# Kernel tuning notes

Hardware: AMD Instinct MI355X
Metric: run time of the kernel (lower is better)

Reference implementation:

```python
import jax, jax.numpy as jnp
import numpy as np

B, T, NF, C, H, TOPK = 4, 8, 8192, 384, 12, 32
D = C // H
SCALE = D ** -0.5  # qk_scale=None -> head_dim**-0.5


def setup_inputs() -> dict:
    key = jax.random.key(0)
    ks = jax.random.split(key, 4)
    x = jax.random.normal(ks[0], (B, T + NF, C), jnp.float32)
    qs_w = jax.random.normal(ks[1], (T, C, C), jnp.float32) * (C ** -0.5)
    kv_w = jax.random.normal(ks[2], (C, 2 * C), jnp.float32) * (C ** -0.5)
    experts_w = jax.random.normal(ks[3], (T, C, C), jnp.float32) * (C ** -0.5)
    return {"x": x, "qs_w": qs_w, "kv_w": kv_w, "experts_w": experts_w}


def reference(x, qs_w, kv_w, experts_w):
    # x: [B, T+NF, C]; first T tokens are task tokens, rest are feature tokens
    feature = x[:, T:, :]                                          # [B,NF,C]
    kv = (feature @ kv_w).reshape(B, NF, 2, H, D)                  # out dim splits [2,H,D]
    k = kv[:, :, 0].transpose(0, 2, 1, 3)                          # [B,H,NF,D]
    v = kv[:, :, 1].transpose(0, 2, 1, 3)                          # [B,H,NF,D]
    # per-task query linears (no bias), one task token each
    q = jnp.einsum('btc,tco->bto', x[:, :T, :], qs_w)              # [B,T,C]
    q = q.reshape(B, T, H, D).transpose(0, 2, 1, 3)                # [B,H,T,D]
    attn = jnp.einsum('bhtd,bhnd->bhtn', q, k) * SCALE             # [B,H,T,NF]
    vals, idx = jax.lax.top_k(attn, TOPK)                          # [B,H,T,K]
    w = jax.nn.softmax(vals, axis=-1)                              # softmax over top-k only
    # attn_token = (scatter(topk softmax) @ v) == weighted gather of v rows
    v_g = jnp.take_along_axis(v[:, :, None], idx[..., None], axis=3)   # [B,H,T,K,D]
    attn_token = jnp.einsum('bhtk,bhtkd->bhtd', w, v_g)
    attn_token = attn_token.transpose(0, 2, 1, 3).reshape(B, T, C)     # [B,T,C]
    # gather raw feature tokens at top-k indices, weight, scatter into padded zeros
    fm = feature.reshape(B, NF, H, D).transpose(0, 2, 1, 3)        # [B,H,NF,D]
    f_g = jnp.take_along_axis(fm[:, :, None], idx[..., None], axis=3) * w[..., None]  # [B,H,T,K,D]
    bi = jnp.arange(B)[:, None, None, None]
    hi = jnp.arange(H)[None, :, None, None]
    ti = jnp.arange(T)[None, None, :, None]
    # topk indices are unique per row -> set is well-defined
    feature_pad = jnp.zeros((B, H, T, NF, D), x.dtype).at[bi, hi, ti, idx].set(f_g)
    feature_pad = feature_pad.transpose(0, 2, 3, 1, 4).reshape(B, T, NF, C)  # [B,T,NF,C]
    # per-task expert linears; einsum with ones weight == sum over tasks
    feature_out = jnp.einsum('btnc,tco->bno', feature_pad, experts_w)  # [B,NF,C]
    token_out = jnp.einsum('btc,tco->bto', attn_token, experts_w)      # [B,T,C]
    return jnp.concatenate([token_out, feature_out], axis=1)          # [B,T+NF,C]
```

## Files before the change

### kernel.cpp

```cpp
#include <hip/hip_runtime.h>
#include <math.h>

#define B 4
#define T 8
#define NF 8192
#define C 384
#define H 12
#define TOPK 32
#define D 32
#define STOT (T + NF)
#define R (H * T)
#define KSEL 48
#define SCALE 0.17677669529663687f

typedef unsigned int uint;
typedef unsigned short ushort;
typedef short bf16x8 __attribute__((ext_vector_type(8)));
typedef float f32x4 __attribute__((ext_vector_type(4)));

__device__ __forceinline__ uint pk_bf16(float a, float b) {
  uint ua = __builtin_bit_cast(uint, a);
  uint ub = __builtin_bit_cast(uint, b);
  ua = (ua + 0x7FFFu + ((ua >> 16) & 1u)) >> 16;
  ub = (ub + 0x7FFFu + ((ub >> 16) & 1u)) >> 16;
  return ua | (ub << 16);
}

__device__ __forceinline__ ushort f32_key(float s) {
  uint u = __builtin_bit_cast(uint, s);
  uint ub = (u + 0x7FFFu + ((u >> 16) & 1u)) >> 16;
  ub ^= (ub & 0x8000u) ? 0xFFFFu : 0x8000u;
  return (ushort)ub;
}

__global__ __launch_bounds__(256) void ta_qproj_kernel(
    const float* __restrict__ x, const float* __restrict__ qs_w,
    float* __restrict__ q_part) {
  int t = blockIdx.x;
  int o0 = blockIdx.y * 64;
  int z = blockIdx.z;
  int tid = threadIdx.x;
  int o = tid & 63, ks = tid >> 6;
  __shared__ float xs[B][192];
  __shared__ float part[4][B][64];
  if (tid < 192) {
    int b = tid / 48, j4 = (tid % 48) * 4;
    *reinterpret_cast<float4*>(&xs[b][j4]) =
        *reinterpret_cast<const float4*>(x + ((size_t)b * STOT + t) * C + z * 192 + j4);
  }
  __syncthreads();
  float a0 = 0.f, a1 = 0.f, a2 = 0.f, a3 = 0.f;
  const float* w = qs_w + (size_t)t * C * C + (size_t)(z * 192 + ks * 48) * C + o0 + o;
#pragma unroll 8
  for (int c = 0; c < 48; ++c) {
    float wv = w[(size_t)c * C];
    int cj = ks * 48 + c;
    a0 += xs[0][cj] * wv;
    a1 += xs[1][cj] * wv;
    a2 += xs[2][cj] * wv;
    a3 += xs[3][cj] * wv;
  }
  part[ks][0][o] = a0; part[ks][1][o] = a1;
  part[ks][2][o] = a2; part[ks][3][o] = a3;
  __syncthreads();
  {
    int b = tid >> 6, oo = tid & 63;
    float s = part[0][b][oo] + part[1][b][oo] + part[2][b][oo] + part[3][b][oo];
    q_part[(((size_t)z * B + b) * T + t) * C + o0 + oo] = s;
  }
}

__global__ __launch_bounds__(384) void ta_fold_kernel(
    const float* __restrict__ q_part, const float* __restrict__ kv_w,
    float* __restrict__ qk_f32, ushort* __restrict__ qk_bf) {
  int b = blockIdx.x / H, h = blockIdx.x % H;
  int tid = threadIdx.x;
  __shared__ float kS[C][33];
  __shared__ float qh[T][D];
  if (tid < T * D) {
    int t = tid >> 5, d = tid & 31;
    qh[t][d] = q_part[((size_t)b * T + t) * C + h * D + d] +
               q_part[(((size_t)B + b) * T + t) * C + h * D + d];
  }
  for (int j = tid; j < C * 8; j += 384) {
    int c = j >> 3, d4 = (j & 7) * 4;
    float4 v = *reinterpret_cast<const float4*>(
        kv_w + (size_t)c * (2 * C) + h * D + d4);
    kS[c][d4 + 0] = v.x; kS[c][d4 + 1] = v.y;
    kS[c][d4 + 2] = v.z; kS[c][d4 + 3] = v.w;
  }
  __syncthreads();
  float acc[T] = {0.f, 0.f, 0.f, 0.f, 0.f, 0.f, 0.f, 0.f};
#pragma unroll
  for (int d = 0; d < D; ++d) {
    float kv = kS[tid][d];
#pragma unroll
    for (int t = 0; t < T; ++t) acc[t] += qh[t][d] * kv;
  }
#pragma unroll
  for (int t = 0; t < T; ++t) {
    size_t off = ((size_t)b * R + (size_t)h * T + t) * C + tid;
    float a = acc[t];
    qk_f32[off] = a;
    uint ua = __builtin_bit_cast(uint, a);
    qk_bf[off] = (ushort)((ua + 0x7FFFu + ((ua >> 16) & 1u)) >> 16);
  }
}

__global__ __launch_bounds__(256) void ta_scores_kernel(
    const float* __restrict__ x, const ushort* __restrict__ qk_bf,
    ushort* __restrict__ keys) {
  int b = blockIdx.y;
  int n0 = blockIdx.x * 64;
  int tid = threadIdx.x;
  int lane = tid & 63, w = tid >> 6;
  int row16 = lane & 15, kg = lane >> 4;
  __shared__ ushort fS[64][72];
  __shared__ ushort qS[96][72];
  f32x4 acc[6];
#pragma unroll
  for (int i = 0; i < 6; ++i) acc[i] = (f32x4){0.f, 0.f, 0.f, 0.f};

  const float* xb = x + ((size_t)b * STOT + T + n0) * C;
  const ushort* qb = qk_bf + (size_t)b * R * C;

  int frow = tid >> 2, fcg = (tid & 3) * 8;

#pragma unroll 1
  for (int c0 = 0; c0 < C; c0 += 32) {
    {
      const float* src = xb + (size_t)frow * C + c0 + fcg;
      float4 v0 = *reinterpret_cast<const float4*>(src);
      float4 v1 = *reinterpret_cast<const float4*>(src + 4);
      uint4 p;
      p.x = pk_bf16(v0.x, v0.y);
      p.y = pk_bf16(v0.z, v0.w);
      p.z = pk_bf16(v1.x, v1.y);
      p.w = pk_bf16(v1.z, v1.w);
      *reinterpret_cast<uint4*>(&fS[frow][fcg]) = p;
    }
#pragma unroll
    for (int s = 0; s < 2; ++s) {
      int u = tid + 256 * s;
      if (u < 384) {
        int row = u >> 2, cg = (u & 3) * 8;
        uint4 v = *reinterpret_cast<const uint4*>(qb + (size_t)row * C + c0 + cg);
        *reinterpret_cast<uint4*>(&qS[row][cg]) = v;
      }
    }
    __syncthreads();
    bf16x8 bfr = *reinterpret_cast<const bf16x8*>(&fS[w * 16 + row16][kg * 8]);
#pragma unroll
    for (int i = 0; i < 6; ++i) {
      bf16x8 afr = *reinterpret_cast<const bf16x8*>(&qS[i * 16 + row16][kg * 8]);
      acc[i] = __builtin_amdgcn_mfma_f32_16x16x32_bf16(afr, bfr, acc[i], 0, 0, 0);
    }
    __syncthreads();
  }
  int n = n0 + w * 16 + row16;
#pragma unroll
  for (int i = 0; i < 6; ++i) {
    int rbase = i * 16 + kg * 4;
#pragma unroll
    for (int reg = 0; reg < 4; ++reg) {
      keys[((size_t)b * R + rbase + reg) * NF + n] = f32_key(acc[i][reg] * SCALE);
    }
  }
}

__global__ __launch_bounds__(384) void ta_selres_kernel(
    const ushort* __restrict__ keys, const float* __restrict__ x,
    const float* __restrict__ qk_f32, float* __restrict__ w_buf,
    int* __restrict__ idx_buf) {
  int rr = blockIdx.x;
  int b = rr / R;
  int tid = threadIdx.x;
  __shared__ __align__(16) ushort su[NF];
  __shared__ uint hist[256], cum[256];
  __shared__ uint sh_prefix, sh_above, cgt, ceq;
  __shared__ int gt_list[KSEL];
  __shared__ int eq_list[128];
  __shared__ int il[KSEL];
  __shared__ float sv[KSEL];
  __shared__ int rkS[KSEL];
  __shared__ float qS[C];
  __shared__ float smax, esum;

  {
    const uint4* src = reinterpret_cast<const uint4*>(keys + (size_t)rr * NF);
    uint4* dst = reinterpret_cast<uint4*>(su);
    for (int j = tid; j < NF / 8; j += 384) dst[j] = src[j];
  }
  qS[tid] = qk_f32[(size_t)rr * C + tid];
  if (tid < 256) hist[tid] = 0;
  if (tid == 0) { cgt = 0; ceq = 0; }
  __syncthreads();

  for (int i = tid; i < NF; i += 384) atomicAdd(&hist[su[i] >> 8], 1u);
  __syncthreads();
  if (tid < 256) cum[tid] = hist[tid];
  __syncthreads();
#pragma unroll
  for (int off = 1; off < 256; off <<= 1) {
    uint add = (tid < 256 - off) ? cum[tid + off] : 0u;
    __syncthreads();
    if (tid < 256) cum[tid] += add;
    __syncthreads();
  }
  if (tid < 256) {
    uint ge = cum[tid], gn = (tid < 255) ? cum[tid + 1] : 0u;
    if (ge >= (uint)KSEL && gn < (uint)KSEL) { sh_prefix = (uint)tid; sh_above = gn; }
  }
  __syncthreads();
  uint pref1 = sh_prefix, ab1 = sh_above;
  if (tid < 256) hist[tid] = 0;
  __syncthreads();
  for (int i = tid; i < NF; i += 384) {
    uint u = su[i];
    if ((u >> 8) == pref1) atomicAdd(&hist[u & 255], 1u);
  }
  __syncthreads();
  if (tid < 256) cum[tid] = hist[tid];
  __syncthreads();
#pragma unroll
  for (int off = 1; off < 256; off <<= 1) {
    uint add = (tid < 256 - off) ? cum[tid + off] : 0u;
    __syncthreads();
    if (tid < 256) cum[tid] += add;
    __syncthreads();
  }
  {
    uint need2 = (uint)KSEL - ab1;
    if (tid < 256) {
      uint ge = cum[tid], gn = (tid < 255) ? cum[tid + 1] : 0u;
      if (ge >= need2 && gn < need2) {
        sh_prefix = (pref1 << 8) | (uint)tid;
        sh_above = ab1 + gn;
      }
    }
  }
  __syncthreads();
  uint piv = sh_prefix, ab = sh_above;
  for (int i = tid; i < NF; i += 384) {
    uint u = su[i];
    if (u > piv) {
      uint s = atomicAdd(&cgt, 1u);
      gt_list[s] = i;
    } else if (u == piv) {
      uint s = atomicAdd(&ceq, 1u);
      if (s < 128) eq_list[s] = i;
    }
  }
  __syncthreads();
  if (tid < (int)ab) il[tid] = gt_list[tid];
  {
    uint ne = ceq < 128u ? ceq : 128u;
    if (tid < (int)ne) {
      int my = eq_list[tid];
      int r2 = 0;
      for (uint e = 0; e < ne; ++e) r2 += (eq_list[e] < my);
      if (r2 < (int)((uint)KSEL - ab)) il[ab + r2] = my;
    }
  }
  __syncthreads();

  int k = tid >> 3, j = tid & 7;
  const float* fp = x + ((size_t)b * STOT + T + il[k]) * C + j;
  float s = 0.f;
#pragma unroll 8
  for (int m = 0; m < 48; ++m) s += fp[m * 8] * qS[j + m * 8];
  s += __shfl_down(s, 4);
  s += __shfl_down(s, 2);
  s += __shfl_down(s, 1);
  if (j == 0) sv[k] = s * SCALE;
  __syncthreads();
  if (tid < KSEL) {
    float mys = sv[tid];
    int myn = il[tid];
    int r = 0;
#pragma unroll
    for (int e = 0; e < KSEL; ++e) {
      float se = sv[e];
      r += (se > mys) || (se == mys && il[e] < myn);
    }
    rkS[tid] = r;
    if (r == 0) smax = mys;
  }
  __syncthreads();
  float e = 0.f;
  if (tid < KSEL && rkS[tid] < TOPK) e = expf(sv[tid] - smax);
  if (tid < 64) {
    float t2 = e;
#pragma unroll
    for (int off = 32; off; off >>= 1) t2 += __shfl_down(t2, off);
    if (tid == 0) esum = t2;
  }
  __syncthreads();
  if (tid < KSEL && rkS[tid] < TOPK) {
    w_buf[(size_t)rr * TOPK + rkS[tid]] = e / esum;
    idx_buf[(size_t)rr * TOPK + rkS[tid]] = il[tid];
  }
}

__global__ __launch_bounds__(256) void ta_zero_kernel(
    float4* __restrict__ out4, int n4) {
  int i = blockIdx.x * 256 + threadIdx.x;
  int stride = gridDim.x * 256;
  float4 z = {0.f, 0.f, 0.f, 0.f};
  for (int j = i; j < n4; j += stride) out4[j] = z;
}

__global__ __launch_bounds__(256) void ta_gv_kernel(
    const float* __restrict__ x, const float* __restrict__ kv_w,
    const float* __restrict__ w_buf, const int* __restrict__ idx_buf,
    float* __restrict__ g_buf, float* __restrict__ att_buf) {
  int br = blockIdx.x;
  int h = (br / T) % H, b = br / R;
  int tid = threadIdx.x;
  int k = tid >> 3, dg = tid & 7;
  __shared__ float Fc[TOPK][100];
  __shared__ float Vc[96][36];
  __shared__ float vS[TOPK][36];
  __shared__ float wl[TOPK];
  __shared__ int il[TOPK];

  if (tid < TOPK) {
    wl[tid] = w_buf[(size_t)br * TOPK + tid];
    il[tid] = idx_buf[(size_t)br * TOPK + tid];
  }
  __syncthreads();
  float4 acc = {0.f, 0.f, 0.f, 0.f};
  int hc = (h * D) / 96;
#pragma unroll 1
  for (int ch = 0; ch < 4; ++ch) {
    int c0 = ch * 96;
    if (ch) __syncthreads();
#pragma unroll
    for (int s = 0; s < 3; ++s) {
      int u = tid + 256 * s;
      int kr = u / 24, c4 = (u % 24) * 4;
      *reinterpret_cast<float4*>(&Fc[kr][c4]) =
          *reinterpret_cast<const float4*>(
              x + ((size_t)b * STOT + T + il[kr]) * C + c0 + c4);
    }
#pragma unroll
    for (int s = 0; s < 3; ++s) {
      int u = tid + 256 * s;
      int cr = u >> 3, d4 = (u & 7) * 4;
      *reinterpret_cast<float4*>(&Vc[cr][d4]) =
          *reinterpret_cast<const float4*>(
              kv_w + (size_t)(c0 + cr) * (2 * C) + C + h * D + d4);
    }
    __syncthreads();
    if (ch == hc) {
      int off = h * D - c0;
      float4 f = *reinterpret_cast<const float4*>(&Fc[k][off + 4 * dg]);
      float wk = wl[k];
      float4 g = {wk * f.x, wk * f.y, wk * f.z, wk * f.w};
      *reinterpret_cast<float4*>(
          &g_buf[((size_t)br * TOPK + k) * D + 4 * dg]) = g;
    }
#pragma unroll 4
    for (int c = 0; c < 96; c += 4) {
      float4 f4 = *reinterpret_cast<const float4*>(&Fc[k][c]);
      float4 v0 = *reinterpret_cast<const float4*>(&Vc[c + 0][4 * dg]);
      float4 v1 = *reinterpret_cast<const float4*>(&Vc[c + 1][4 * dg]);
      float4 v2 = *reinterpret_cast<const float4*>(&Vc[c + 2][4 * dg]);
      float4 v3 = *reinterpret_cast<const float4*>(&Vc[c + 3][4 * dg]);
      acc.x += f4.x * v0.x + f4.y * v1.x + f4.z * v2.x + f4.w * v3.x;
      acc.y += f4.x * v0.y + f4.y * v1.y + f4.z * v2.y + f4.w * v3.y;
      acc.z += f4.x * v0.z + f4.y * v1.z + f4.z * v2.z + f4.w * v3.z;
      acc.w += f4.x * v0.w + f4.y * v1.w + f4.z * v2.w + f4.w * v3.w;
    }
  }
  *reinterpret_cast<float4*>(&vS[k][4 * dg]) = acc;
  __syncthreads();
  if (tid < D) {
    float a = 0.f;
#pragma unroll
    for (int kk = 0; kk < TOPK; ++kk) a += wl[kk] * vS[kk][tid];
    att_buf[(size_t)br * D + tid] = a;
  }
}

__global__ __launch_bounds__(384) void ta_scatter_kernel(
    const float* __restrict__ ew, const float* __restrict__ g_buf,
    const float* __restrict__ att_buf, const int* __restrict__ idx_buf,
    float* __restrict__ out) {
  int grp = blockIdx.x >> 2, b = blockIdx.x & 3;
  int t = grp / H, h = grp % H;
  int br = b * R + h * T + t;
  int tid = threadIdx.x;
  __shared__ float gS[TOPK * D];
  __shared__ __align__(16) float attS[D];
  __shared__ int ilS[TOPK];

  for (int u = tid; u < TOPK * D / 4; u += 384)
    *reinterpret_cast<float4*>(gS + u * 4) =
        *reinterpret_cast<const float4*>(g_buf + (size_t)br * TOPK * D + u * 4);
  if (tid < TOPK) ilS[tid] = idx_buf[(size_t)br * TOPK + tid];
  if (tid < D) attS[tid] = att_buf[(size_t)br * D + tid];
  __syncthreads();

  float ewc[D];
  const float* ewt = ew + (size_t)t * C * C + (size_t)h * D * C + tid;
#pragma unroll
  for (int dd = 0; dd < D; ++dd) ewc[dd] = ewt[(size_t)dd * C];

  size_t obase = (size_t)b * STOT * C + tid;
#pragma unroll 1
  for (int kk = 0; kk < TOPK; ++kk) {
    float y = 0.f;
#pragma unroll
    for (int d4 = 0; d4 < D; d4 += 4) {
      float4 g4 = *reinterpret_cast<const float4*>(gS + kk * D + d4);
      y += g4.x * ewc[d4] + g4.y * ewc[d4 + 1] +
           g4.z * ewc[d4 + 2] + g4.w * ewc[d4 + 3];
    }
    atomicAdd(&out[obase + (size_t)(T + ilS[kk]) * C], y);
  }
  {
    float y = 0.f;
#pragma unroll
    for (int d4 = 0; d4 < D; d4 += 4) {
      float4 a4 = *reinterpret_cast<const float4*>(attS + d4);
      y += a4.x * ewc[d4] + a4.y * ewc[d4 + 1] +
           a4.z * ewc[d4 + 2] + a4.w * ewc[d4 + 3];
    }
    atomicAdd(&out[obase + (size_t)t * C], y);
  }
}

extern "C" void kernel_launch(void* const* d_in, const int* in_sizes, int n_in,
                              void* d_out, int out_size, void* d_ws, size_t ws_size,
                              hipStream_t stream) {
  const float* x = (const float*)d_in[0];
  const float* qs_w = (const float*)d_in[1];
  const float* kv_w = (const float*)d_in[2];
  const float* ew = (const float*)d_in[3];
  float* out = (float*)d_out;

  char* p = (char*)d_ws;
  float* qk_f32 = (float*)p;  p += (size_t)B * R * C * 4;
  ushort* qk_bf = (ushort*)p; p += (size_t)B * R * C * 2;
  ushort* keys = (ushort*)p;  p += (size_t)B * R * NF * 2;
  float* w_buf = (float*)p;   p += (size_t)B * R * TOPK * 4;
  int* idx_buf = (int*)p;     p += (size_t)B * R * TOPK * 4;
  float* g_buf = (float*)p;   p += (size_t)B * R * TOPK * D * 4;
  float* att_buf = (float*)p; p += (size_t)B * R * D * 4;
  float* q_part = (float*)p;

  dim3 gq(T, C / 64, 2);
  ta_qproj_kernel<<<gq, 256, 0, stream>>>(x, qs_w, q_part);
  ta_fold_kernel<<<B * H, 384, 0, stream>>>(q_part, kv_w, qk_f32, qk_bf);
  dim3 g2(NF / 64, B);
  ta_scores_kernel<<<g2, 256, 0, stream>>>(x, qk_bf, keys);
  ta_selres_kernel<<<B * R, 384, 0, stream>>>(keys, x, qk_f32, w_buf, idx_buf);
  ta_zero_kernel<<<2048, 256, 0, stream>>>((float4*)out, out_size / 4);
  ta_gv_kernel<<<B * R, 256, 0, stream>>>(x, kv_w, w_buf, idx_buf, g_buf, att_buf);
  ta_scatter_kernel<<<T * H * B, 384, 0, stream>>>(ew, g_buf, att_buf, idx_buf, out);
}
```

Measured before the change: 97.69 us.

## Fuse zeroing into selection, merge gather and scatter kernels, warp-scan histograms

Output zeroing moves out of its own kernel into the top-k selection kernel, with each block clearing a slice of the output. The gather kernel and the expert scatter kernel are merged, so the weighted feature rows and the attention token stay in shared memory instead of going through global buffers. The radix-select histograms become per-wave copies, summed by one wave with a shuffle-based suffix scan, replacing the barrier-heavy 256-wide scan. Manual bf16 rounding is swapped for the library conversion. Risks: 256-thread blocks now cover 384 columns with uneven per-thread work, and the merged kernel uses more registers.

```diff
diff --git a/kernel.cpp b/kernel.cpp
--- a/kernel.cpp
+++ b/kernel.cpp
@@ -1,4 +1,5 @@
 #include <hip/hip_runtime.h>
+#include <hip/hip_bf16.h>
 #include <math.h>
 
 #define B 4
@@ -18,19 +19,14 @@
 typedef short bf16x8 __attribute__((ext_vector_type(8)));
 typedef float f32x4 __attribute__((ext_vector_type(4)));
 
-__device__ __forceinline__ uint pk_bf16(float a, float b) {
-  uint ua = __builtin_bit_cast(uint, a);
-  uint ub = __builtin_bit_cast(uint, b);
-  ua = (ua + 0x7FFFu + ((ua >> 16) & 1u)) >> 16;
-  ub = (ub + 0x7FFFu + ((ub >> 16) & 1u)) >> 16;
-  return ua | (ub << 16);
+__device__ __forceinline__ ushort bf16u(float a) {
+  return __builtin_bit_cast(ushort, __float2bfloat16(a));
 }
 
 __device__ __forceinline__ ushort f32_key(float s) {
-  uint u = __builtin_bit_cast(uint, s);
-  uint ub = (u + 0x7FFFu + ((u >> 16) & 1u)) >> 16;
-  ub ^= (ub & 0x8000u) ? 0xFFFFu : 0x8000u;
-  return (ushort)ub;
+  uint kb = bf16u(s);
+  kb ^= (kb & 0x8000u) ? 0xFFFFu : 0x8000u;
+  return (ushort)kb;
 }
 
 __global__ __launch_bounds__(256) void ta_qproj_kernel(
@@ -102,8 +98,7 @@
     size_t off = ((size_t)b * R + (size_t)h * T + t) * C + tid;
     float a = acc[t];
     qk_f32[off] = a;
-    uint ua = __builtin_bit_cast(uint, a);
-    qk_bf[off] = (ushort)((ua + 0x7FFFu + ((ua >> 16) & 1u)) >> 16);
+    qk_bf[off] = bf16u(a);
   }
 }
 
@@ -133,10 +128,10 @@
       float4 v0 = *reinterpret_cast<const float4*>(src);
       float4 v1 = *reinterpret_cast<const float4*>(src + 4);
       uint4 p;
-      p.x = pk_bf16(v0.x, v0.y);
-      p.y = pk_bf16(v0.z, v0.w);
-      p.z = pk_bf16(v1.x, v1.y);
-      p.w = pk_bf16(v1.z, v1.w);
+      p.x = (uint)bf16u(v0.x) | ((uint)bf16u(v0.y) << 16);
+      p.y = (uint)bf16u(v0.z) | ((uint)bf16u(v0.w) << 16);
+      p.z = (uint)bf16u(v1.x) | ((uint)bf16u(v1.y) << 16);
+      p.w = (uint)bf16u(v1.z) | ((uint)bf16u(v1.w) << 16);
       *reinterpret_cast<uint4*>(&fS[frow][fcg]) = p;
     }
 #pragma unroll
@@ -171,12 +166,13 @@
 __global__ __launch_bounds__(384) void ta_selres_kernel(
     const ushort* __restrict__ keys, const float* __restrict__ x,
     const float* __restrict__ qk_f32, float* __restrict__ w_buf,
-    int* __restrict__ idx_buf) {
+    int* __restrict__ idx_buf, float4* __restrict__ out4) {
   int rr = blockIdx.x;
   int b = rr / R;
   int tid = threadIdx.x;
+  int lane = tid & 63, wvi = tid >> 6;
   __shared__ __align__(16) ushort su[NF];
-  __shared__ uint hist[256], cum[256];
+  __shared__ uint histW[6][256];
   __shared__ uint sh_prefix, sh_above, cgt, ceq;
   __shared__ int gt_list[KSEL];
   __shared__ int eq_list[128];
@@ -191,53 +187,80 @@
     uint4* dst = reinterpret_cast<uint4*>(su);
     for (int j = tid; j < NF / 8; j += 384) dst[j] = src[j];
   }
+  {
+    float4 z = {0.f, 0.f, 0.f, 0.f};
+    float4* dst = out4 + (size_t)rr * (B * STOT * C / 4 / (B * R));
+    for (int j = tid; j < B * STOT * C / 4 / (B * R); j += 384) dst[j] = z;
+  }
   qS[tid] = qk_f32[(size_t)rr * C + tid];
-  if (tid < 256) hist[tid] = 0;
+  for (int i = tid; i < 6 * 256; i += 384) (&histW[0][0])[i] = 0;
   if (tid == 0) { cgt = 0; ceq = 0; }
   __syncthreads();
 
-  for (int i = tid; i < NF; i += 384) atomicAdd(&hist[su[i] >> 8], 1u);
-  __syncthreads();
-  if (tid < 256) cum[tid] = hist[tid];
-  __syncthreads();
-#pragma unroll
-  for (int off = 1; off < 256; off <<= 1) {
-    uint add = (tid < 256 - off) ? cum[tid + off] : 0u;
-    __syncthreads();
-    if (tid < 256) cum[tid] += add;
-    __syncthreads();
-  }
-  if (tid < 256) {
-    uint ge = cum[tid], gn = (tid < 255) ? cum[tid + 1] : 0u;
-    if (ge >= (uint)KSEL && gn < (uint)KSEL) { sh_prefix = (uint)tid; sh_above = gn; }
+  for (int i = tid; i < NF; i += 384) atomicAdd(&histW[wvi][su[i] >> 8], 1u);
+  __syncthreads();
+  if (tid < 64) {
+    uint h0 = 0, h1 = 0, h2 = 0, h3 = 0;
+#pragma unroll
+    for (int wq = 0; wq < 6; ++wq) {
+      h0 += histW[wq][4 * lane + 0];
+      h1 += histW[wq][4 * lane + 1];
+      h2 += histW[wq][4 * lane + 2];
+      h3 += histW[wq][4 * lane + 3];
+    }
+    uint lsum = h0 + h1 + h2 + h3;
+    uint suf = lsum;
+#pragma unroll
+    for (int off = 1; off < 64; off <<= 1) {
+      uint o = __shfl_down(suf, off);
+      if (lane + off < 64) suf += o;
+    }
+    uint gn3 = suf - lsum;
+    uint ge3 = gn3 + h3;
+    uint ge2 = ge3 + h2;
+    uint ge1 = ge2 + h1;
+    uint ge0 = ge1 + h0;
+    const uint need = KSEL;
+    if (ge0 >= need && ge1 < need) { sh_prefix = 4 * lane + 0; sh_above = ge1; }
+    if (ge1 >= need && ge2 < need) { sh_prefix = 4 * lane + 1; sh_above = ge2; }
+    if (ge2 >= need && ge3 < need) { sh_prefix = 4 * lane + 2; sh_above = ge3; }
+    if (ge3 >= need && gn3 < need) { sh_prefix = 4 * lane + 3; sh_above = gn3; }
   }
   __syncthreads();
   uint pref1 = sh_prefix, ab1 = sh_above;
-  if (tid < 256) hist[tid] = 0;
+  for (int i = tid; i < 6 * 256; i += 384) (&histW[0][0])[i] = 0;
   __syncthreads();
   for (int i = tid; i < NF; i += 384) {
     uint u = su[i];
-    if ((u >> 8) == pref1) atomicAdd(&hist[u & 255], 1u);
-  }
-  __syncthreads();
-  if (tid < 256) cum[tid] = hist[tid];
-  __syncthreads();
-#pragma unroll
-  for (int off = 1; off < 256; off <<= 1) {
-    uint add = (tid < 256 - off) ? cum[tid + off] : 0u;
-    __syncthreads();
-    if (tid < 256) cum[tid] += add;
-    __syncthreads();
-  }
-  {
-    uint need2 = (uint)KSEL - ab1;
-    if (tid < 256) {
-      uint ge = cum[tid], gn = (tid < 255) ? cum[tid + 1] : 0u;
-      if (ge >= need2 && gn < need2) {
-        sh_prefix = (pref1 << 8) | (uint)tid;
-        sh_above = ab1 + gn;
-      }
-    }
+    if ((u >> 8) == pref1) atomicAdd(&histW[wvi][u & 255], 1u);
+  }
+  __syncthreads();
+  if (tid < 64) {
+    uint h0 = 0, h1 = 0, h2 = 0, h3 = 0;
+#pragma unroll
+    for (int wq = 0; wq < 6; ++wq) {
+      h0 += histW[wq][4 * lane + 0];
+      h1 += histW[wq][4 * lane + 1];
+      h2 += histW[wq][4 * lane + 2];
+      h3 += histW[wq][4 * lane + 3];
+    }
+    uint lsum = h0 + h1 + h2 + h3;
+    uint suf = lsum;
+#pragma unroll
+    for (int off = 1; off < 64; off <<= 1) {
+      uint o = __shfl_down(suf, off);
+      if (lane + off < 64) suf += o;
+    }
+    uint gn3 = suf - lsum;
+    uint ge3 = gn3 + h3;
+    uint ge2 = ge3 + h2;
+    uint ge1 = ge2 + h1;
+    uint ge0 = ge1 + h0;
+    const uint need = (uint)KSEL - ab1;
+    if (ge0 >= need && ge1 < need) { sh_prefix = (pref1 << 8) | (4 * lane + 0); sh_above = ab1 + ge1; }
+    if (ge1 >= need && ge2 < need) { sh_prefix = (pref1 << 8) | (4 * lane + 1); sh_above = ab1 + ge2; }
+    if (ge2 >= need && ge3 < need) { sh_prefix = (pref1 << 8) | (4 * lane + 2); sh_above = ab1 + ge3; }
+    if (ge3 >= need && gn3 < need) { sh_prefix = (pref1 << 8) | (4 * lane + 3); sh_above = ab1 + gn3; }
   }
   __syncthreads();
   uint piv = sh_prefix, ab = sh_above;
@@ -302,25 +325,19 @@
   }
 }
 
-__global__ __launch_bounds__(256) void ta_zero_kernel(
-    float4* __restrict__ out4, int n4) {
-  int i = blockIdx.x * 256 + threadIdx.x;
-  int stride = gridDim.x * 256;
-  float4 z = {0.f, 0.f, 0.f, 0.f};
-  for (int j = i; j < n4; j += stride) out4[j] = z;
-}
-
-__global__ __launch_bounds__(256) void ta_gv_kernel(
+__global__ __launch_bounds__(256) void ta_gvscatter_kernel(
     const float* __restrict__ x, const float* __restrict__ kv_w,
-    const float* __restrict__ w_buf, const int* __restrict__ idx_buf,
-    float* __restrict__ g_buf, float* __restrict__ att_buf) {
+    const float* __restrict__ ew, const float* __restrict__ w_buf,
+    const int* __restrict__ idx_buf, float* __restrict__ out) {
   int br = blockIdx.x;
-  int h = (br / T) % H, b = br / R;
+  int t = br % T, h = (br / T) % H, b = br / R;
   int tid = threadIdx.x;
   int k = tid >> 3, dg = tid & 7;
   __shared__ float Fc[TOPK][100];
   __shared__ float Vc[96][36];
   __shared__ float vS[TOPK][36];
+  __shared__ float gS[TOPK][36];
+  __shared__ __align__(16) float attS[D];
   __shared__ float wl[TOPK];
   __shared__ int il[TOPK];
 
@@ -357,8 +374,7 @@
       float4 f = *reinterpret_cast<const float4*>(&Fc[k][off + 4 * dg]);
       float wk = wl[k];
       float4 g = {wk * f.x, wk * f.y, wk * f.z, wk * f.w};
-      *reinterpret_cast<float4*>(
-          &g_buf[((size_t)br * TOPK + k) * D + 4 * dg]) = g;
+      *reinterpret_cast<float4*>(&gS[k][4 * dg]) = g;
     }
 #pragma unroll 4
     for (int c = 0; c < 96; c += 4) {
@@ -379,55 +395,46 @@
     float a = 0.f;
 #pragma unroll
     for (int kk = 0; kk < TOPK; ++kk) a += wl[kk] * vS[kk][tid];
-    att_buf[(size_t)br * D + tid] = a;
-  }
-}
-
-__global__ __launch_bounds__(384) void ta_scatter_kernel(
-    const float* __restrict__ ew, const float* __restrict__ g_buf,
-    const float* __restrict__ att_buf, const int* __restrict__ idx_buf,
-    float* __restrict__ out) {
-  int grp = blockIdx.x >> 2, b = blockIdx.x & 3;
-  int t = grp / H, h = grp % H;
-  int br = b * R + h * T + t;
-  int tid = threadIdx.x;
-  __shared__ float gS[TOPK * D];
-  __shared__ __align__(16) float attS[D];
-  __shared__ int ilS[TOPK];
-
-  for (int u = tid; u < TOPK * D / 4; u += 384)
-    *reinterpret_cast<float4*>(gS + u * 4) =
-        *reinterpret_cast<const float4*>(g_buf + (size_t)br * TOPK * D + u * 4);
-  if (tid < TOPK) ilS[tid] = idx_buf[(size_t)br * TOPK + tid];
-  if (tid < D) attS[tid] = att_buf[(size_t)br * D + tid];
-  __syncthreads();
-
-  float ewc[D];
-  const float* ewt = ew + (size_t)t * C * C + (size_t)h * D * C + tid;
-#pragma unroll
-  for (int dd = 0; dd < D; ++dd) ewc[dd] = ewt[(size_t)dd * C];
-
-  size_t obase = (size_t)b * STOT * C + tid;
+    attS[tid] = a;
+  }
+  __syncthreads();
+
+  float ewc0[D], ewc1[D];
+  const float* ewt = ew + (size_t)t * C * C + (size_t)h * D * C;
+#pragma unroll
+  for (int dd = 0; dd < D; ++dd) {
+    ewc0[dd] = ewt[(size_t)dd * C + tid];
+    ewc1[dd] = (tid < 128) ? ewt[(size_t)dd * C + tid + 256] : 0.f;
+  }
+  size_t obase = (size_t)b * STOT * C;
 #pragma unroll 1
   for (int kk = 0; kk < TOPK; ++kk) {
-    float y = 0.f;
+    float y0 = 0.f, y1 = 0.f;
 #pragma unroll
     for (int d4 = 0; d4 < D; d4 += 4) {
-      float4 g4 = *reinterpret_cast<const float4*>(gS + kk * D + d4);
-      y += g4.x * ewc[d4] + g4.y * ewc[d4 + 1] +
-           g4.z * ewc[d4 + 2] + g4.w * ewc[d4 + 3];
-    }
-    atomicAdd(&out[obase + (size_t)(T + ilS[kk]) * C], y);
+      float4 g4 = *reinterpret_cast<const float4*>(&gS[kk][d4]);
+      y0 += g4.x * ewc0[d4] + g4.y * ewc0[d4 + 1] +
+            g4.z * ewc0[d4 + 2] + g4.w * ewc0[d4 + 3];
+      y1 += g4.x * ewc1[d4] + g4.y * ewc1[d4 + 1] +
+            g4.z * ewc1[d4 + 2] + g4.w * ewc1[d4 + 3];
+    }
+    size_t row = obase + (size_t)(T + il[kk]) * C;
+    atomicAdd(&out[row + tid], y0);
+    if (tid < 128) atomicAdd(&out[row + tid + 256], y1);
   }
   {
-    float y = 0.f;
+    float y0 = 0.f, y1 = 0.f;
 #pragma unroll
     for (int d4 = 0; d4 < D; d4 += 4) {
       float4 a4 = *reinterpret_cast<const float4*>(attS + d4);
-      y += a4.x * ewc[d4] + a4.y * ewc[d4 + 1] +
-           a4.z * ewc[d4 + 2] + a4.w * ewc[d4 + 3];
-    }
-    atomicAdd(&out[obase + (size_t)t * C], y);
+      y0 += a4.x * ewc0[d4] + a4.y * ewc0[d4 + 1] +
+            a4.z * ewc0[d4 + 2] + a4.w * ewc0[d4 + 3];
+      y1 += a4.x * ewc1[d4] + a4.y * ewc1[d4 + 1] +
+            a4.z * ewc1[d4 + 2] + a4.w * ewc1[d4 + 3];
+    }
+    size_t row = obase + (size_t)t * C;
+    atomicAdd(&out[row + tid], y0);
+    if (tid < 128) atomicAdd(&out[row + tid + 256], y1);
   }
 }
 
@@ -446,8 +453,6 @@
   ushort* keys = (ushort*)p;  p += (size_t)B * R * NF * 2;
   float* w_buf = (float*)p;   p += (size_t)B * R * TOPK * 4;
   int* idx_buf = (int*)p;     p += (size_t)B * R * TOPK * 4;
-  float* g_buf = (float*)p;   p += (size_t)B * R * TOPK * D * 4;
-  float* att_buf = (float*)p; p += (size_t)B * R * D * 4;
   float* q_part = (float*)p;
 
   dim3 gq(T, C / 64, 2);
@@ -455,8 +460,7 @@
   ta_fold_kernel<<<B * H, 384, 0, stream>>>(q_part, kv_w, qk_f32, qk_bf);
   dim3 g2(NF / 64, B);
   ta_scores_kernel<<<g2, 256, 0, stream>>>(x, qk_bf, keys);
-  ta_selres_kernel<<<B * R, 384, 0, stream>>>(keys, x, qk_f32, w_buf, idx_buf);
-  ta_zero_kernel<<<2048, 256, 0, stream>>>((float4*)out, out_size / 4);
-  ta_gv_kernel<<<B * R, 256, 0, stream>>>(x, kv_w, w_buf, idx_buf, g_buf, att_buf);
-  ta_scatter_kernel<<<T * H * B, 384, 0, stream>>>(ew, g_buf, att_buf, idx_buf, out);
-}
+  ta_selres_kernel<<<B * R, 384, 0, stream>>>(keys, x, qk_f32, w_buf, idx_buf,
+                                              (float4*)out);
+  ta_gvscatter_kernel<<<B * R, 256, 0, stream>>>(x, kv_w, ew, w_buf, idx_buf, out);
+}
```

After: 88.77 us. 1.1x faster.
